# Kernel tuning notes

Measured on AMD Instinct MI355X. Metric: run time of the kernel, lower is better.

Reference implementation:

```python
import jax, jax.numpy as jnp
import numpy as np

B, V, N, C, H = 4, 8, 256, 768, 12
DH = C // H
NEG = -1e9


def setup_inputs() -> dict:
    key = jax.random.key(0)
    k0, k1, k2, k3, k4, k5 = jax.random.split(key, 6)
    feats = jax.random.normal(k0, (B, V, N, C), dtype=jnp.float32)
    is_ref = jax.random.randint(k1, (B, V), 0, 2).astype(bool)
    # nn.MultiheadAttention params: packed in_proj (3C, C) + bias, out_proj Linear(C, C)
    w_qkv = jax.random.normal(k2, (3 * C, C), dtype=jnp.float32) * 0.02
    b_qkv = jax.random.normal(k3, (3 * C,), dtype=jnp.float32) * 0.02
    w_out = jax.random.normal(k4, (C, C), dtype=jnp.float32) * 0.02
    b_out = jax.random.normal(k5, (C,), dtype=jnp.float32) * 0.02
    return {"feats": feats, "is_ref": is_ref, "w_qkv": w_qkv, "b_qkv": b_qkv,
            "w_out": w_out, "b_out": b_out}


def reference(feats, is_ref, w_qkv, b_qkv, w_out, b_out):
    b_, v_, n_, c_ = feats.shape
    # packed QKV projection (torch Linear: x @ W.T + b)
    qkv = feats @ w_qkv.T + b_qkv                      # (B,V,N,3C)
    q, k, v = jnp.split(qkv, 3, axis=-1)
    q = q.reshape(b_, v_, n_, H, DH) * (1.0 / jnp.sqrt(jnp.float32(DH)))
    k = k.reshape(b_, v_ * n_, H, DH)                  # keys flattened over views
    v = v.reshape(b_, v_ * n_, H, DH)
    # view v attends to views w with opposite ref flag
    allowed = is_ref[:, :, None] ^ is_ref[:, None, :]  # (B,V,V) bool
    key_mask = jnp.repeat(allowed, n_, axis=2)         # (B,V,V*N)
    scores = jnp.einsum('bvnhd,bmhd->bhvnm', q, k)     # (B,H,V,N,V*N)
    logits = jnp.where(key_mask[:, None, :, None, :], scores, NEG)
    attn = jax.nn.softmax(logits, axis=-1)
    ctx = jnp.einsum('bhvnm,bmhd->bvnhd', attn, v).reshape(b_, v_, n_, c_)
    out = ctx @ w_out.T + b_out
    # views with empty context pass through unchanged
    has_ctx = allowed.any(axis=-1)                     # (B,V)
    return jnp.where(has_ctx[:, :, None, None], out, feats)
```

## Files before the change

### kernel.cpp

```cpp
#include <hip/hip_runtime.h>
#include <hip/hip_bf16.h>
#include <math.h>

#define BDIM 4
#define VDIM 8
#define NDIM 256
#define CDIM 768
#define HDIM 12
#define DHE  64
#define C3   (3*CDIM)
#define ROWS (BDIM*VDIM*NDIM)
#define KEYS (VDIM*NDIM)

typedef __attribute__((ext_vector_type(8))) short short8;
typedef __attribute__((ext_vector_type(4))) float float4v;

__device__ __forceinline__ unsigned int pk2(float a, float b) {
    unsigned int r;
    asm("v_cvt_pk_bf16_f32 %0, %1, %2" : "=v"(r) : "v"(a), "v"(b));
    return r;
}

__device__ __forceinline__ uint4 pk8(float4 a, float4 b) {
    uint4 r;
    r.x = pk2(a.x, a.y); r.y = pk2(a.z, a.w);
    r.z = pk2(b.x, b.y); r.w = pk2(b.z, b.w);
    return r;
}

__device__ __forceinline__ void gld_lds16(const unsigned short* g, unsigned short* l) {
    __builtin_amdgcn_global_load_lds(
        (const __attribute__((address_space(1))) void*)g,
        (__attribute__((address_space(3))) void*)l, 16, 0, 0);
}

#define QSCALE 0.18033688f

#define NA8 786432
#define NW8 221184
#define NO8 73728

__global__ __launch_bounds__(256) void cast_bf16_all(
    const float* __restrict__ fA, const float* __restrict__ fW,
    const float* __restrict__ fO,
    unsigned short* __restrict__ bA, unsigned short* __restrict__ bW,
    unsigned short* __restrict__ bO)
{
    const int gid = blockIdx.x * 256 + threadIdx.x;
    const float* src;
    unsigned short* dst;
    int idx;
    if (gid < NA8)            { src = fA; dst = bA; idx = gid; }
    else if (gid < NA8 + NW8) { src = fW; dst = bW; idx = gid - NA8; }
    else                      { src = fO; dst = bO; idx = gid - NA8 - NW8; }
    const float4* p = (const float4*)(src + (size_t)idx * 8);
    *(uint4*)(dst + (size_t)idx * 8) = pk8(p[0], p[1]);
}

__global__ __launch_bounds__(256) void gemm_qkv_mfma(
    const unsigned short* __restrict__ A,
    const unsigned short* __restrict__ W,
    const float* __restrict__ bias,
    unsigned short* __restrict__ out,
    unsigned short* __restrict__ vT)
{
    __shared__ __attribute__((aligned(16))) unsigned short As[2][128][32];
    __shared__ __attribute__((aligned(16))) unsigned short Ws[2][128][32];
    const int t = threadIdx.x;
    const int wave = t >> 6, lane = t & 63;
    const int m = lane & 15, quad = lane >> 4;
    const int wr = (wave >> 1) * 64, wc = (wave & 1) * 64;

    const int lin = blockIdx.y * gridDim.x + blockIdx.x;
    const int cpx = (gridDim.x * gridDim.y) >> 3;
    const int swz = (lin & 7) * cpx + (lin >> 3);
    const int row0 = (swz / gridDim.x) * 128, col0 = (swz % gridDim.x) * 128;

    const int sr = t >> 2, sk = (t & 3) * 8;
    const unsigned short* ag = &A[(size_t)(row0 + sr) * CDIM + sk];
    const unsigned short* wg = &W[(size_t)(col0 + sr) * CDIM + sk];

    float4v acc[4][4] = {};

    for (int k0 = 0; k0 < CDIM; k0 += 64) {
        #pragma unroll
        for (int ks = 0; ks < 2; ks++) {
            gld_lds16(ag + k0 + ks * 32, &As[ks][sr][sk]);
            gld_lds16(ag + (size_t)64 * CDIM + k0 + ks * 32, &As[ks][64 + sr][sk]);
            gld_lds16(wg + k0 + ks * 32, &Ws[ks][sr][sk]);
            gld_lds16(wg + (size_t)64 * CDIM + k0 + ks * 32, &Ws[ks][64 + sr][sk]);
        }
        __syncthreads();
        #pragma unroll
        for (int ks = 0; ks < 2; ks++) {
            short8 a[4], b[4];
            #pragma unroll
            for (int rt = 0; rt < 4; rt++)
                a[rt] = *(const short8*)&As[ks][wr + rt * 16 + m][quad * 8];
            #pragma unroll
            for (int ct = 0; ct < 4; ct++)
                b[ct] = *(const short8*)&Ws[ks][wc + ct * 16 + m][quad * 8];
            #pragma unroll
            for (int rt = 0; rt < 4; rt++)
                #pragma unroll
                for (int ct = 0; ct < 4; ct++)
                    acc[rt][ct] = __builtin_amdgcn_mfma_f32_16x16x32_bf16(
                        a[rt], b[ct], acc[rt][ct], 0, 0, 0);
        }
        __syncthreads();
    }

    if (col0 < 2 * CDIM) {
        const float qs = (col0 < CDIM) ? QSCALE : 1.0f;
        #pragma unroll
        for (int ct = 0; ct < 4; ct++) {
            const int col = col0 + wc + ct * 16 + m;
            const float bv = bias[col];
            #pragma unroll
            for (int rt = 0; rt < 4; rt++) {
                const size_t row = (size_t)row0 + wr + rt * 16 + quad * 4;
                const unsigned u01 = pk2((acc[rt][ct][0] + bv) * qs,
                                         (acc[rt][ct][1] + bv) * qs);
                const unsigned u23 = pk2((acc[rt][ct][2] + bv) * qs,
                                         (acc[rt][ct][3] + bv) * qs);
                out[(row + 0) * C3 + col] = (unsigned short)u01;
                out[(row + 1) * C3 + col] = (unsigned short)(u01 >> 16);
                out[(row + 2) * C3 + col] = (unsigned short)u23;
                out[(row + 3) * C3 + col] = (unsigned short)(u23 >> 16);
            }
        }
    } else {
        #pragma unroll
        for (int ct = 0; ct < 4; ct++) {
            const int vcol = col0 + wc + ct * 16 + m - 2 * CDIM;
            const int h = vcol >> 6, d = vcol & 63;
            const float bv = bias[col0 + wc + ct * 16 + m];
            #pragma unroll
            for (int rt = 0; rt < 4; rt++) {
                const int row = row0 + wr + rt * 16 + quad * 4;
                const int bidx = row >> 11, key = row & 2047;
                uint2 pv2;
                pv2.x = pk2(acc[rt][ct][0] + bv, acc[rt][ct][1] + bv);
                pv2.y = pk2(acc[rt][ct][2] + bv, acc[rt][ct][3] + bv);
                *(uint2*)&vT[((size_t)(bidx * HDIM + h) * DHE + d) * KEYS + key] = pv2;
            }
        }
    }
}

__global__ __launch_bounds__(256, 3) void attn_mfma(
    const unsigned short* __restrict__ qkv,
    const unsigned short* __restrict__ vT,
    const int* __restrict__ is_ref,
    unsigned short* __restrict__ ctx)
{
    const int g = blockIdx.x;
    const int myx = g & 7, cuu = (g >> 3) & 31, round = g >> 8;
    const int j = round * 32 + ((round & 1) ? (31 - cuu) : cuu);

    int rmask[4], r4[4];
    #pragma unroll
    for (int bb = 0; bb < 4; bb++) {
        int mask = 0;
        #pragma unroll
        for (int w = 0; w < VDIM; w++)
            if (is_ref[bb * VDIM + w] != 0) mask |= 1 << w;
        rmask[bb] = mask; r4[bb] = __popc(mask);
    }
    int ord[4] = {0, 1, 2, 3};
    #pragma unroll
    for (int i = 0; i < 3; i++)
        #pragma unroll
        for (int k = 0; k < 3 - i; k++) {
            const int wa = r4[ord[k]] * (8 - r4[ord[k]]);
            const int wb = r4[ord[k + 1]] * (8 - r4[ord[k + 1]]);
            if (wb > wa) { int tmp = ord[k]; ord[k] = ord[k + 1]; ord[k + 1] = tmp; }
        }
    int Gb[6], Gh[6], ng = 0;
    for (int p = 0; p < 48; p++) {
        const int row = p >> 3, col = p & 7;
        const int x = (row & 1) ? (7 - col) : col;
        if (x == myx) { Gb[ng] = ord[p / 12]; Gh[ng] = p % 12; ng++; }
    }
    int b = 0, h = 0, half = 0, v = 0, Lsel = 0;
    {
        int jj = j;
        bool found = false;
        for (int o = 8; o >= 0 && !found; o--) {
            for (int gi = 0; gi < 6 && !found; gi++) {
                const int b2 = Gb[gi], r2 = r4[b2];
                const int nv_o = ((8 - r2) == o ? r2 : 0) + (r2 == o ? (8 - r2) : 0);
                const int cnt = 2 * nv_o;
                if (cnt > 0 && jj < cnt) {
                    b = b2; h = Gh[gi]; Lsel = o;
                    half = jj / nv_o;
                    int pos = jj % nv_o;
                    int S = (((8 - r2) == o) ? rmask[b2] : 0)
                          | ((r2 == o) ? ((~rmask[b2]) & 0xff) : 0);
                    for (int vv = 0; vv < 8; vv++)
                        if ((S >> vv) & 1) { if (pos == 0) { v = vv; break; } pos--; }
                    found = true;
                } else jj -= cnt;
            }
        }
    }

    const int t = threadIdx.x, wave = t >> 6, lane = t & 63;
    const int m = lane & 15, quad = lane >> 4;
    const int n0 = half * 128 + wave * 32;

    __shared__ unsigned short Ks[2][64][64];
    __shared__ unsigned short Vs[2][64][64];
    __shared__ unsigned short Ps[4][32][72];

    const int my_ref = (rmask[b] >> v) & 1;
    const unsigned amask = my_ref ? (unsigned)((~rmask[b]) & 0xff)
                                  : (unsigned)rmask[b];
    const int nC = 4 * Lsel;

    unsigned vpack = 0;
    {
        unsigned rm = amask; int pi = 0;
        while (rm) { vpack |= (unsigned)(__builtin_ffs((int)rm) - 1) << (4 * pi);
                     rm &= rm - 1; pi++; }
    }

    short8 aq[2][2];
    #pragma unroll
    for (int qt = 0; qt < 2; qt++) {
        const size_t row = (size_t)((b * VDIM + v) * NDIM) + n0 + qt * 16 + m;
        #pragma unroll
        for (int ks = 0; ks < 2; ks++)
            aq[qt][ks] = *(const short8*)&qkv[row * C3 + h * DHE + ks * 32 + quad * 8];
    }

    float rs[2] = {0.f, 0.f};
    float4v O[2][4] = {};

    const int s_row = t >> 2;
    const int s_g   = (t & 3) * 2;

    const unsigned short* vTb = vT + (size_t)(b * HDIM + h) * DHE * KEYS;
    const unsigned short* qkb = qkv + (size_t)(b * VDIM) * NDIM * C3 + CDIM + h * DHE;

    uint4 kreg[2], vreg[2];

    #define LOADC(c)                                                           \
        {                                                                      \
            const int w_ = (int)((vpack >> (((c) >> 2) * 4)) & 15);            \
            const int kb_ = ((c) & 3) * 64;                                    \
            const unsigned short* kp = qkb + (size_t)(w_ * NDIM + kb_ + s_row) * C3; \
            kreg[0] = *(const uint4*)&kp[(s_g + 0) * 8];                       \
            kreg[1] = *(const uint4*)&kp[(s_g + 1) * 8];                       \
            const unsigned short* vp = vTb + (size_t)s_row * KEYS + w_ * NDIM + kb_; \
            vreg[0] = *(const uint4*)&vp[(s_g + 0) * 8];                       \
            vreg[1] = *(const uint4*)&vp[(s_g + 1) * 8];                       \
        }
    #define WRITEC(buf)                                                        \
        {                                                                      \
            *(uint4*)&Ks[buf][s_row][((s_g + 0) ^ (s_row & 7)) * 8] = kreg[0]; \
            *(uint4*)&Ks[buf][s_row][((s_g + 1) ^ (s_row & 7)) * 8] = kreg[1]; \
            *(uint4*)&Vs[buf][s_row][((s_g + 0) ^ (s_row & 7)) * 8] = vreg[0]; \
            *(uint4*)&Vs[buf][s_row][((s_g + 1) ^ (s_row & 7)) * 8] = vreg[1]; \
        }

    if (nC > 0) {
        LOADC(0);
        WRITEC(0);
        if (nC > 1) LOADC(1);
    }

    for (int c = 0; c < nC; c++) {
        const int buf = c & 1;
        __syncthreads();
        if (c + 1 < nC) {
            WRITEC(buf ^ 1);
            if (c + 2 < nC) LOADC(c + 2);
        }

        #pragma unroll
        for (int kt = 0; kt < 4; kt++) {
            const short8 bk0 = *(const short8*)&Ks[buf][kt * 16 + m][(quad ^ (m & 7)) * 8];
            const short8 bk1 = *(const short8*)&Ks[buf][kt * 16 + m][((4 + quad) ^ (m & 7)) * 8];
            #pragma unroll
            for (int qt = 0; qt < 2; qt++) {
                float4v s = {};
                s = __builtin_amdgcn_mfma_f32_16x16x32_bf16(bk0, aq[qt][0], s, 0, 0, 0);
                s = __builtin_amdgcn_mfma_f32_16x16x32_bf16(bk1, aq[qt][1], s, 0, 0, 0);
                const float p0 = __builtin_amdgcn_exp2f(s[0]);
                const float p1 = __builtin_amdgcn_exp2f(s[1]);
                const float p2 = __builtin_amdgcn_exp2f(s[2]);
                const float p3 = __builtin_amdgcn_exp2f(s[3]);
                rs[qt] += (p0 + p1) + (p2 + p3);
                uint2 pw;
                pw.x = pk2(p0, p1);
                pw.y = pk2(p2, p3);
                *(uint2*)&Ps[wave][qt * 16 + m][kt * 16 + quad * 4] = pw;
            }
        }
        #pragma unroll
        for (int kk = 0; kk < 2; kk++) {
            const short8 ap0 = *(const short8*)&Ps[wave][m][kk * 32 + quad * 8];
            const short8 ap1 = *(const short8*)&Ps[wave][16 + m][kk * 32 + quad * 8];
            #pragma unroll
            for (int ct = 0; ct < 4; ct++) {
                const short8 bv = *(const short8*)&Vs[buf][ct * 16 + m]
                    [((kk * 4 + quad) ^ (m & 7)) * 8];
                O[0][ct] = __builtin_amdgcn_mfma_f32_16x16x32_bf16(ap0, bv, O[0][ct], 0, 0, 0);
                O[1][ct] = __builtin_amdgcn_mfma_f32_16x16x32_bf16(ap1, bv, O[1][ct], 0, 0, 0);
            }
        }
    }
    #undef LOADC
    #undef WRITEC

    #pragma unroll
    for (int qt = 0; qt < 2; qt++) {
        float x = rs[qt];
        x += __shfl_xor(x, 16, 64);
        x += __shfl_xor(x, 32, 64);
        const float inv = (x > 0.f) ? 1.f / x : 0.f;
        float invq[4];
        #pragma unroll
        for (int r = 0; r < 4; r++)
            invq[r] = __shfl(inv, quad * 4 + r, 64);
        const size_t rowg = (size_t)((b * VDIM + v) * NDIM) + n0 + qt * 16 + quad * 4;
        #pragma unroll
        for (int ct = 0; ct < 4; ct++) {
            const int cc = h * DHE + ct * 16 + m;
            const unsigned u01 = pk2(O[qt][ct][0] * invq[0], O[qt][ct][1] * invq[1]);
            const unsigned u23 = pk2(O[qt][ct][2] * invq[2], O[qt][ct][3] * invq[3]);
            ctx[(rowg + 0) * CDIM + cc] = (unsigned short)u01;
            ctx[(rowg + 1) * CDIM + cc] = (unsigned short)(u01 >> 16);
            ctx[(rowg + 2) * CDIM + cc] = (unsigned short)u23;
            ctx[(rowg + 3) * CDIM + cc] = (unsigned short)(u23 >> 16);
        }
    }
}

__global__ __launch_bounds__(256) void gemm_out_mfma(
    const unsigned short* __restrict__ A,
    const unsigned short* __restrict__ W,
    const float* __restrict__ bias,
    const float* __restrict__ feats,
    const int* __restrict__ is_ref,
    float* __restrict__ out)
{
    __shared__ __attribute__((aligned(16))) unsigned short As[2][128][32];
    __shared__ __attribute__((aligned(16))) unsigned short Ws[2][128][32];
    const int t = threadIdx.x;
    const int wave = t >> 6, lane = t & 63;
    const int m = lane & 15, quad = lane >> 4;
    const int wr = (wave >> 1) * 64, wc = (wave & 1) * 64;

    const int lin = blockIdx.y * gridDim.x + blockIdx.x;
    const int cpx = (gridDim.x * gridDim.y) >> 3;
    const int swz = (lin & 7) * cpx + (lin >> 3);
    const int row0 = (swz / gridDim.x) * 128, col0 = (swz % gridDim.x) * 128;

    const int sr = t >> 2, sk = (t & 3) * 8;
    const unsigned short* ag = &A[(size_t)(row0 + sr) * CDIM + sk];
    const unsigned short* wg = &W[(size_t)(col0 + sr) * CDIM + sk];

    float4v acc[4][4] = {};

    for (int k0 = 0; k0 < CDIM; k0 += 64) {
        #pragma unroll
        for (int ks = 0; ks < 2; ks++) {
            gld_lds16(ag + k0 + ks * 32, &As[ks][sr][sk]);
            gld_lds16(ag + (size_t)64 * CDIM + k0 + ks * 32, &As[ks][64 + sr][sk]);
            gld_lds16(wg + k0 + ks * 32, &Ws[ks][sr][sk]);
            gld_lds16(wg + (size_t)64 * CDIM + k0 + ks * 32, &Ws[ks][64 + sr][sk]);
        }
        __syncthreads();
        #pragma unroll
        for (int ks = 0; ks < 2; ks++) {
            short8 a[4], b[4];
            #pragma unroll
            for (int rt = 0; rt < 4; rt++)
                a[rt] = *(const short8*)&As[ks][wr + rt * 16 + m][quad * 8];
            #pragma unroll
            for (int ct = 0; ct < 4; ct++)
                b[ct] = *(const short8*)&Ws[ks][wc + ct * 16 + m][quad * 8];
            #pragma unroll
            for (int rt = 0; rt < 4; rt++)
                #pragma unroll
                for (int ct = 0; ct < 4; ct++)
                    acc[rt][ct] = __builtin_amdgcn_mfma_f32_16x16x32_bf16(
                        a[rt], b[ct], acc[rt][ct], 0, 0, 0);
        }
        __syncthreads();
    }

    const int bidx = row0 / (VDIM * NDIM);
    const int vidx = (row0 / NDIM) % VDIM;
    const int my = is_ref[bidx * VDIM + vidx];
    bool has = false;
    #pragma unroll
    for (int w = 0; w < VDIM; w++) has = has || (is_ref[bidx * VDIM + w] != my);

    #pragma unroll
    for (int ct = 0; ct < 4; ct++) {
        const int col = col0 + wc + ct * 16 + m;
        const float bv = bias[col];
        #pragma unroll
        for (int rt = 0; rt < 4; rt++) {
            const size_t row = (size_t)row0 + wr + rt * 16 + quad * 4;
            #pragma unroll
            for (int r = 0; r < 4; r++) {
                float o = acc[rt][ct][r] + bv;
                if (!has) o = feats[(row + r) * CDIM + col];
                out[(row + r) * CDIM + col] = o;
            }
        }
    }
}

extern "C" void kernel_launch(void* const* d_in, const int* in_sizes, int n_in,
                              void* d_out, int out_size, void* d_ws, size_t ws_size,
                              hipStream_t stream) {
    const float* feats = (const float*)d_in[0];
    const int*   is_ref = (const int*)d_in[1];
    const float* w_qkv = (const float*)d_in[2];
    const float* b_qkv = (const float*)d_in[3];
    const float* w_out = (const float*)d_in[4];
    const float* b_out = (const float*)d_in[5];
    float* out = (float*)d_out;

    unsigned short* qkv_b = (unsigned short*)d_ws;
    unsigned short* vT    = qkv_b + (size_t)ROWS * C3;
    unsigned short* ctx_b = vT + (size_t)BDIM * HDIM * DHE * KEYS;
    unsigned short* A_bf  = ctx_b + (size_t)ROWS * CDIM;
    unsigned short* Wq_bf = A_bf + (size_t)ROWS * CDIM;
    unsigned short* Wo_bf = Wq_bf + (size_t)C3 * CDIM;

    cast_bf16_all<<<dim3((NA8 + NW8 + NO8) / 256), 256, 0, stream>>>(
        feats, w_qkv, w_out, A_bf, Wq_bf, Wo_bf);

    dim3 g1(C3 / 128, ROWS / 128);
    gemm_qkv_mfma<<<g1, 256, 0, stream>>>(A_bf, Wq_bf, b_qkv, qkv_b, vT);

    attn_mfma<<<dim3(768), 256, 0, stream>>>(qkv_b, vT, is_ref, ctx_b);

    dim3 g3(CDIM / 128, ROWS / 128);
    gemm_out_mfma<<<g3, 256, 0, stream>>>(ctx_b, Wo_bf, b_out, feats, is_ref, out);
    (void)in_sizes; (void)n_in; (void)out_size; (void)ws_size;
}
```

Before: 222.7 us.

## Load K fragments directly into registers with two-stage prefetch instead of LDS

The attention inner loop no longer stages K tiles through shared memory. Each wave loads its K MFMA fragments straight from global memory into two register buffers, prefetched two chunks ahead, and the loop is unrolled by two to alternate between them. This removes the LDS writes and reads for K and shrinks shared memory use. In exchange, each of the four waves fetches the same K data, with strided 16-byte accesses, and register pressure rises.

```diff
diff --git a/kernel.cpp b/kernel.cpp
--- a/kernel.cpp
+++ b/kernel.cpp
@@ -209,7 +209,6 @@
     const int m = lane & 15, quad = lane >> 4;
     const int n0 = half * 128 + wave * 32;
 
-    __shared__ unsigned short Ks[2][64][64];
     __shared__ unsigned short Vs[2][64][64];
     __shared__ unsigned short Ps[4][32][72];
 
@@ -243,76 +242,93 @@
     const unsigned short* vTb = vT + (size_t)(b * HDIM + h) * DHE * KEYS;
     const unsigned short* qkb = qkv + (size_t)(b * VDIM) * NDIM * C3 + CDIM + h * DHE;
 
-    uint4 kreg[2], vreg[2];
-
-    #define LOADC(c)                                                           \
+    uint4 vreg[2];
+    uint4 kfA[4][2], kfB[4][2];
+
+    #define LOADV(c)                                                           \
         {                                                                      \
             const int w_ = (int)((vpack >> (((c) >> 2) * 4)) & 15);            \
             const int kb_ = ((c) & 3) * 64;                                    \
-            const unsigned short* kp = qkb + (size_t)(w_ * NDIM + kb_ + s_row) * C3; \
-            kreg[0] = *(const uint4*)&kp[(s_g + 0) * 8];                       \
-            kreg[1] = *(const uint4*)&kp[(s_g + 1) * 8];                       \
             const unsigned short* vp = vTb + (size_t)s_row * KEYS + w_ * NDIM + kb_; \
             vreg[0] = *(const uint4*)&vp[(s_g + 0) * 8];                       \
             vreg[1] = *(const uint4*)&vp[(s_g + 1) * 8];                       \
         }
-    #define WRITEC(buf)                                                        \
+    #define WRITEV(buf)                                                        \
         {                                                                      \
-            *(uint4*)&Ks[buf][s_row][((s_g + 0) ^ (s_row & 7)) * 8] = kreg[0]; \
-            *(uint4*)&Ks[buf][s_row][((s_g + 1) ^ (s_row & 7)) * 8] = kreg[1]; \
             *(uint4*)&Vs[buf][s_row][((s_g + 0) ^ (s_row & 7)) * 8] = vreg[0]; \
             *(uint4*)&Vs[buf][s_row][((s_g + 1) ^ (s_row & 7)) * 8] = vreg[1]; \
         }
+    #define LOADKF(c, kf)                                                      \
+        {                                                                      \
+            const int w_ = (int)((vpack >> (((c) >> 2) * 4)) & 15);            \
+            const unsigned short* kp = qkb                                     \
+                + (size_t)(w_ * NDIM + ((c) & 3) * 64) * C3;                   \
+            _Pragma("unroll")                                                  \
+            for (int nt = 0; nt < 4; nt++)                                     \
+                _Pragma("unroll")                                              \
+                for (int ks = 0; ks < 2; ks++)                                 \
+                    kf[nt][ks] = *(const uint4*)&kp[(size_t)(nt * 16 + m) * C3 \
+                                                    + ks * 32 + quad * 8];     \
+        }
+    #define WINDOW(c, cur)                                                     \
+        {                                                                      \
+            const int buf = (c) & 1;                                           \
+            __syncthreads();                                                   \
+            if ((c) + 1 < nC) {                                                \
+                WRITEV(buf ^ 1);                                               \
+                if ((c) + 2 < nC) LOADV((c) + 2);                              \
+            }                                                                  \
+            _Pragma("unroll")                                                  \
+            for (int kt = 0; kt < 4; kt++) {                                   \
+                const short8 bk0 = __builtin_bit_cast(short8, cur[kt][0]);     \
+                const short8 bk1 = __builtin_bit_cast(short8, cur[kt][1]);     \
+                _Pragma("unroll")                                              \
+                for (int qt = 0; qt < 2; qt++) {                               \
+                    float4v s = {};                                            \
+                    s = __builtin_amdgcn_mfma_f32_16x16x32_bf16(bk0, aq[qt][0], s, 0, 0, 0); \
+                    s = __builtin_amdgcn_mfma_f32_16x16x32_bf16(bk1, aq[qt][1], s, 0, 0, 0); \
+                    const float p0 = __builtin_amdgcn_exp2f(s[0]);             \
+                    const float p1 = __builtin_amdgcn_exp2f(s[1]);             \
+                    const float p2 = __builtin_amdgcn_exp2f(s[2]);             \
+                    const float p3 = __builtin_amdgcn_exp2f(s[3]);             \
+                    rs[qt] += (p0 + p1) + (p2 + p3);                           \
+                    uint2 pw;                                                  \
+                    pw.x = pk2(p0, p1);                                        \
+                    pw.y = pk2(p2, p3);                                        \
+                    *(uint2*)&Ps[wave][qt * 16 + m][kt * 16 + quad * 4] = pw;  \
+                }                                                              \
+            }                                                                  \
+            if ((c) + 2 < nC) LOADKF((c) + 2, cur);                            \
+            _Pragma("unroll")                                                  \
+            for (int kk = 0; kk < 2; kk++) {                                   \
+                const short8 ap0 = *(const short8*)&Ps[wave][m][kk * 32 + quad * 8]; \
+                const short8 ap1 = *(const short8*)&Ps[wave][16 + m][kk * 32 + quad * 8]; \
+                _Pragma("unroll")                                              \
+                for (int ct = 0; ct < 4; ct++) {                               \
+                    const short8 bv = *(const short8*)&Vs[buf][ct * 16 + m]    \
+                        [((kk * 4 + quad) ^ (m & 7)) * 8];                     \
+                    O[0][ct] = __builtin_amdgcn_mfma_f32_16x16x32_bf16(ap0, bv, O[0][ct], 0, 0, 0); \
+                    O[1][ct] = __builtin_amdgcn_mfma_f32_16x16x32_bf16(ap1, bv, O[1][ct], 0, 0, 0); \
+                }                                                              \
+            }                                                                  \
+        }
 
     if (nC > 0) {
-        LOADC(0);
-        WRITEC(0);
-        if (nC > 1) LOADC(1);
-    }
-
-    for (int c = 0; c < nC; c++) {
-        const int buf = c & 1;
-        __syncthreads();
-        if (c + 1 < nC) {
-            WRITEC(buf ^ 1);
-            if (c + 2 < nC) LOADC(c + 2);
-        }
-
-        #pragma unroll
-        for (int kt = 0; kt < 4; kt++) {
-            const short8 bk0 = *(const short8*)&Ks[buf][kt * 16 + m][(quad ^ (m & 7)) * 8];
-            const short8 bk1 = *(const short8*)&Ks[buf][kt * 16 + m][((4 + quad) ^ (m & 7)) * 8];
-            #pragma unroll
-            for (int qt = 0; qt < 2; qt++) {
-                float4v s = {};
-                s = __builtin_amdgcn_mfma_f32_16x16x32_bf16(bk0, aq[qt][0], s, 0, 0, 0);
-                s = __builtin_amdgcn_mfma_f32_16x16x32_bf16(bk1, aq[qt][1], s, 0, 0, 0);
-                const float p0 = __builtin_amdgcn_exp2f(s[0]);
-                const float p1 = __builtin_amdgcn_exp2f(s[1]);
-                const float p2 = __builtin_amdgcn_exp2f(s[2]);
-                const float p3 = __builtin_amdgcn_exp2f(s[3]);
-                rs[qt] += (p0 + p1) + (p2 + p3);
-                uint2 pw;
-                pw.x = pk2(p0, p1);
-                pw.y = pk2(p2, p3);
-                *(uint2*)&Ps[wave][qt * 16 + m][kt * 16 + quad * 4] = pw;
-            }
-        }
-        #pragma unroll
-        for (int kk = 0; kk < 2; kk++) {
-            const short8 ap0 = *(const short8*)&Ps[wave][m][kk * 32 + quad * 8];
-            const short8 ap1 = *(const short8*)&Ps[wave][16 + m][kk * 32 + quad * 8];
-            #pragma unroll
-            for (int ct = 0; ct < 4; ct++) {
-                const short8 bv = *(const short8*)&Vs[buf][ct * 16 + m]
-                    [((kk * 4 + quad) ^ (m & 7)) * 8];
-                O[0][ct] = __builtin_amdgcn_mfma_f32_16x16x32_bf16(ap0, bv, O[0][ct], 0, 0, 0);
-                O[1][ct] = __builtin_amdgcn_mfma_f32_16x16x32_bf16(ap1, bv, O[1][ct], 0, 0, 0);
-            }
-        }
-    }
-    #undef LOADC
-    #undef WRITEC
+        LOADV(0);
+        WRITEV(0);
+        if (nC > 1) LOADV(1);
+        LOADKF(0, kfA);
+        if (nC > 1) LOADKF(1, kfB);
+    }
+
+    for (int c = 0; c < nC; c += 2) {
+        WINDOW(c, kfA);
+        WINDOW(c + 1, kfB);
+    }
+    #undef LOADV
+    #undef WRITEV
+    #undef LOADKF
+    #undef WINDOW
 
     #pragma unroll
     for (int qt = 0; qt < 2; qt++) {
```

Result: slower. 292.0 us (+31.1%).

## Double-buffer LDS staging in QKV and output GEMMs to overlap loads with MFMA

Applied to the files above, without the earlier changes.

Both bf16 GEMM kernels now stream the K dimension in 32-wide slices through two LDS buffers. The next slice's global-to-LDS load is issued right after the barrier, before the MFMAs on the current slice run. Each slice needs one barrier instead of two, so the memory latency of each load can hide behind the previous slice's compute. In exchange, each MFMA batch is smaller, and correctness depends on the barrier also waiting for the outstanding async LDS loads.

```diff
diff --git a/kernel.cpp b/kernel.cpp
--- a/kernel.cpp
+++ b/kernel.cpp
@@ -80,35 +80,36 @@
     const unsigned short* ag = &A[(size_t)(row0 + sr) * CDIM + sk];
     const unsigned short* wg = &W[(size_t)(col0 + sr) * CDIM + sk];
 
+    #define STAGE(k0, bf)                                                  \
+        {                                                                  \
+            gld_lds16(ag + (k0), &As[bf][sr][sk]);                         \
+            gld_lds16(ag + (size_t)64 * CDIM + (k0), &As[bf][64 + sr][sk]);\
+            gld_lds16(wg + (k0), &Ws[bf][sr][sk]);                         \
+            gld_lds16(wg + (size_t)64 * CDIM + (k0), &Ws[bf][64 + sr][sk]);\
+        }
+
     float4v acc[4][4] = {};
 
-    for (int k0 = 0; k0 < CDIM; k0 += 64) {
-        #pragma unroll
-        for (int ks = 0; ks < 2; ks++) {
-            gld_lds16(ag + k0 + ks * 32, &As[ks][sr][sk]);
-            gld_lds16(ag + (size_t)64 * CDIM + k0 + ks * 32, &As[ks][64 + sr][sk]);
-            gld_lds16(wg + k0 + ks * 32, &Ws[ks][sr][sk]);
-            gld_lds16(wg + (size_t)64 * CDIM + k0 + ks * 32, &Ws[ks][64 + sr][sk]);
-        }
+    STAGE(0, 0);
+    for (int k = 0; k < CDIM / 32; k++) {
+        const int bf = k & 1;
         __syncthreads();
-        #pragma unroll
-        for (int ks = 0; ks < 2; ks++) {
-            short8 a[4], b[4];
-            #pragma unroll
-            for (int rt = 0; rt < 4; rt++)
-                a[rt] = *(const short8*)&As[ks][wr + rt * 16 + m][quad * 8];
+        if (k + 1 < CDIM / 32) STAGE((k + 1) * 32, bf ^ 1);
+        short8 a[4], b[4];
+        #pragma unroll
+        for (int rt = 0; rt < 4; rt++)
+            a[rt] = *(const short8*)&As[bf][wr + rt * 16 + m][quad * 8];
+        #pragma unroll
+        for (int ct = 0; ct < 4; ct++)
+            b[ct] = *(const short8*)&Ws[bf][wc + ct * 16 + m][quad * 8];
+        #pragma unroll
+        for (int rt = 0; rt < 4; rt++)
             #pragma unroll
             for (int ct = 0; ct < 4; ct++)
-                b[ct] = *(const short8*)&Ws[ks][wc + ct * 16 + m][quad * 8];
-            #pragma unroll
-            for (int rt = 0; rt < 4; rt++)
-                #pragma unroll
-                for (int ct = 0; ct < 4; ct++)
-                    acc[rt][ct] = __builtin_amdgcn_mfma_f32_16x16x32_bf16(
-                        a[rt], b[ct], acc[rt][ct], 0, 0, 0);
-        }
-        __syncthreads();
-    }
+                acc[rt][ct] = __builtin_amdgcn_mfma_f32_16x16x32_bf16(
+                    a[rt], b[ct], acc[rt][ct], 0, 0, 0);
+    }
+    #undef STAGE
 
     if (col0 < 2 * CDIM) {
         const float qs = (col0 < CDIM) ? QSCALE : 1.0f;
@@ -362,35 +363,36 @@
     const unsigned short* ag = &A[(size_t)(row0 + sr) * CDIM + sk];
     const unsigned short* wg = &W[(size_t)(col0 + sr) * CDIM + sk];
 
+    #define STAGE(k0, bf)                                                  \
+        {                                                                  \
+            gld_lds16(ag + (k0), &As[bf][sr][sk]);                         \
+            gld_lds16(ag + (size_t)64 * CDIM + (k0), &As[bf][64 + sr][sk]);\
+            gld_lds16(wg + (k0), &Ws[bf][sr][sk]);                         \
+            gld_lds16(wg + (size_t)64 * CDIM + (k0), &Ws[bf][64 + sr][sk]);\
+        }
+
     float4v acc[4][4] = {};
 
-    for (int k0 = 0; k0 < CDIM; k0 += 64) {
-        #pragma unroll
-        for (int ks = 0; ks < 2; ks++) {
-            gld_lds16(ag + k0 + ks * 32, &As[ks][sr][sk]);
-            gld_lds16(ag + (size_t)64 * CDIM + k0 + ks * 32, &As[ks][64 + sr][sk]);
-            gld_lds16(wg + k0 + ks * 32, &Ws[ks][sr][sk]);
-            gld_lds16(wg + (size_t)64 * CDIM + k0 + ks * 32, &Ws[ks][64 + sr][sk]);
-        }
+    STAGE(0, 0);
+    for (int k = 0; k < CDIM / 32; k++) {
+        const int bf = k & 1;
         __syncthreads();
-        #pragma unroll
-        for (int ks = 0; ks < 2; ks++) {
-            short8 a[4], b[4];
-            #pragma unroll
-            for (int rt = 0; rt < 4; rt++)
-                a[rt] = *(const short8*)&As[ks][wr + rt * 16 + m][quad * 8];
+        if (k + 1 < CDIM / 32) STAGE((k + 1) * 32, bf ^ 1);
+        short8 a[4], b[4];
+        #pragma unroll
+        for (int rt = 0; rt < 4; rt++)
+            a[rt] = *(const short8*)&As[bf][wr + rt * 16 + m][quad * 8];
+        #pragma unroll
+        for (int ct = 0; ct < 4; ct++)
+            b[ct] = *(const short8*)&Ws[bf][wc + ct * 16 + m][quad * 8];
+        #pragma unroll
+        for (int rt = 0; rt < 4; rt++)
             #pragma unroll
             for (int ct = 0; ct < 4; ct++)
-                b[ct] = *(const short8*)&Ws[ks][wc + ct * 16 + m][quad * 8];
-            #pragma unroll
-            for (int rt = 0; rt < 4; rt++)
-                #pragma unroll
-                for (int ct = 0; ct < 4; ct++)
-                    acc[rt][ct] = __builtin_amdgcn_mfma_f32_16x16x32_bf16(
-                        a[rt], b[ct], acc[rt][ct], 0, 0, 0);
-        }
-        __syncthreads();
-    }
+                acc[rt][ct] = __builtin_amdgcn_mfma_f32_16x16x32_bf16(
+                    a[rt], b[ct], acc[rt][ct], 0, 0, 0);
+    }
+    #undef STAGE
 
     const int bidx = row0 / (VDIM * NDIM);
     const int vidx = (row0 / NDIM) % VDIM;
```

Result: slower. 239.3 us (+7.5%).
